# Kernel optimization log

Measured on AMD Instinct MI355X. Metric: run time of the kernel, lower is better.

Reference implementation:

```python
import jax, jax.numpy as jnp
import numpy as np

N_NODES = 100000
N_EDGES = 1600000
IN_FEATS = 256
OUT_FEATS = 128
GAMMA = 1.0


def setup_inputs() -> dict:
    key = jax.random.key(0)
    k1, k2, k3, k4, k5 = jax.random.split(key, 5)
    glorot = np.sqrt(6.0 / (IN_FEATS + OUT_FEATS)).astype(np.float32)
    feat = jax.random.normal(k1, (N_NODES, IN_FEATS), dtype=jnp.float32)
    W_mean = jax.random.uniform(k2, (IN_FEATS, OUT_FEATS), dtype=jnp.float32, minval=-glorot, maxval=glorot)
    W_var = jax.random.uniform(k3, (IN_FEATS, OUT_FEATS), dtype=jnp.float32, minval=-glorot, maxval=glorot)
    src = jax.random.randint(k4, (N_EDGES,), 0, N_NODES, dtype=jnp.int64 if jax.config.jax_enable_x64 else jnp.int32)
    dst = jax.random.randint(k5, (N_EDGES,), 0, N_NODES, dtype=jnp.int64 if jax.config.jax_enable_x64 else jnp.int32)
    return {"feat": feat, "W_mean": W_mean, "W_var": W_var, "src": src, "dst": dst}


def reference(feat, W_mean, W_var, src, dst):
    # dense projections + relu (no bias, as bias=False)
    mean = jax.nn.relu(jnp.matmul(feat, W_mean))   # [N, F]
    var = jax.nn.relu(jnp.matmul(feat, W_var))     # [N, F]
    attention = jnp.exp(-GAMMA * var)
    # in-degrees from dst edge endpoints, clamped to >= 1
    degs = jax.ops.segment_sum(jnp.ones_like(dst, dtype=jnp.float32), dst, num_segments=N_NODES)
    degs = jnp.clip(degs, 1.0)
    norm1 = (degs ** -0.5)[:, None]                # [N, 1] = D^{-1/2}
    norm2 = norm1 * norm1                          # [N, 1] = D^{-1}
    m_msg = mean * attention * norm1
    v_msg = var * attention * attention * norm2
    # copy_src + sum aggregation (SpMM over edge list)
    mean_agg = jax.ops.segment_sum(m_msg[src], dst, num_segments=N_NODES) * norm1
    var_agg = jax.ops.segment_sum(v_msg[src], dst, num_segments=N_NODES) * norm2
    return mean_agg, var_agg
```

## Files before the change

kernel.cpp:

```cpp
#include <hip/hip_runtime.h>
#include <hip/hip_bf16.h>

#define N_NODES 100000
#define N_EDGES 1600000
#define OUTF 128
#define INF 256
#define SCAN_CHUNK 1024
#define SCAN_BLOCKS 98
#define M_TILES 6250

typedef _Float16 f16;
typedef _Float16 half8 __attribute__((ext_vector_type(8)));
typedef _Float16 half2v __attribute__((ext_vector_type(2)));
typedef float floatx4 __attribute__((ext_vector_type(4)));

__global__ void count_rank_kernel(const int* __restrict__ dst, int E,
                                  int* __restrict__ deg, int* __restrict__ rank) {
    int i = blockIdx.x * blockDim.x + threadIdx.x;
    if (i < E) rank[i] = atomicAdd(&deg[dst[i]], 1);
}

__global__ __launch_bounds__(256) void scan_partial_kernel(const int* __restrict__ deg, int n,
                                                           int* __restrict__ partial) {
    __shared__ int red[256];
    int b = blockIdx.x, t = threadIdx.x;
    int base = b * SCAN_CHUNK;
    int s = 0;
    for (int i = t; i < SCAN_CHUNK; i += 256) {
        int idx = base + i;
        if (idx < n) s += deg[idx];
    }
    red[t] = s;
    __syncthreads();
    for (int off = 128; off > 0; off >>= 1) {
        if (t < off) red[t] += red[t + off];
        __syncthreads();
    }
    if (t == 0) partial[b] = red[0];
}

__global__ __launch_bounds__(128) void scan_top_kernel(int* __restrict__ partial, int nb,
                                                       int* __restrict__ row_start, int n) {
    __shared__ int sc[128];
    int t = threadIdx.x;
    int v = (t < nb) ? partial[t] : 0;
    sc[t] = v;
    __syncthreads();
    for (int off = 1; off < 128; off <<= 1) {
        int val = sc[t];
        int add = (t >= off) ? sc[t - off] : 0;
        __syncthreads();
        sc[t] = val + add;
        __syncthreads();
    }
    if (t < nb) partial[t] = sc[t] - v;
    if (t == 127) row_start[n] = sc[127];
}

__global__ __launch_bounds__(256) void scan_final_kernel(const int* __restrict__ deg, int n,
                                                         const int* __restrict__ partial,
                                                         int* __restrict__ row_start,
                                                         float* __restrict__ norm1,
                                                         float* __restrict__ norm2) {
    __shared__ int sc[256];
    int b = blockIdx.x, t = threadIdx.x;
    int base = b * SCAN_CHUNK + t * 4;
    int v[4];
    int tsum = 0;
#pragma unroll
    for (int j = 0; j < 4; j++) {
        int idx = base + j;
        v[j] = (idx < n) ? deg[idx] : 0;
        tsum += v[j];
    }
    sc[t] = tsum;
    __syncthreads();
    for (int off = 1; off < 256; off <<= 1) {
        int val = sc[t];
        int add = (t >= off) ? sc[t - off] : 0;
        __syncthreads();
        sc[t] = val + add;
        __syncthreads();
    }
    int run = sc[t] - tsum + partial[b];
#pragma unroll
    for (int j = 0; j < 4; j++) {
        int idx = base + j;
        if (idx < n) {
            row_start[idx] = run;
            float d = (float)(v[j] > 0 ? v[j] : 1);
            norm1[idx] = rsqrtf(d);
            norm2[idx] = 1.0f / d;
            run += v[j];
        }
    }
}

__global__ void scatter_edges_kernel(const int* __restrict__ src, const int* __restrict__ dst,
                                     const int* __restrict__ rank,
                                     const int* __restrict__ row_start,
                                     int E, int* __restrict__ srcs_sorted) {
    int i = blockIdx.x * blockDim.x + threadIdx.x;
    if (i < E) {
        srcs_sorted[row_start[dst[i]] + rank[i]] = src[i];
    }
}

__global__ __launch_bounds__(256) void convert_B_kernel(const float* __restrict__ Wm,
                                                        const float* __restrict__ Wv,
                                                        f16* __restrict__ Bt) {
    int k = threadIdx.x;
    int ng = blockIdx.x;
    int g = ng >> 4, i = ng & 15;
    int w = g >> 2, cg = g & 3;
    int col = w * 32 + (cg & 1) * 16 + i;
    const float* srcW = (cg >= 2) ? Wv : Wm;
    Bt[ng * 256 + k] = (f16)srcW[k * 128 + col];
}

__global__ __launch_bounds__(256, 2) void proj_mfma_kernel(const float* __restrict__ feat,
                                                           const f16* __restrict__ Bt,
                                                           const float* __restrict__ norm1,
                                                           const float* __restrict__ norm2,
                                                           f16* __restrict__ msg) {
    int tid = threadIdx.x;
    int w = tid >> 6;
    int lane = tid & 63;
    int quad = lane >> 4;
    int l15 = lane & 15;

    half8 b[4][8];
#pragma unroll
    for (int cg = 0; cg < 4; cg++) {
        int g = w * 4 + cg;
        const f16* bp = Bt + (size_t)(g * 16 + l15) * 256 + quad * 8;
#pragma unroll
        for (int kf = 0; kf < 8; kf++) {
            b[cg][kf] = *(const half8*)(bp + kf * 32);
        }
    }

    for (int t = blockIdx.x; t < M_TILES; t += gridDim.x) {
        int m0 = t * 16;
        half8 a[8];
        const float* ap = feat + (size_t)(m0 + l15) * 256 + quad * 8;
#pragma unroll
        for (int kf = 0; kf < 8; kf++) {
            floatx4 f0 = *(const floatx4*)(ap + kf * 32);
            floatx4 f1 = *(const floatx4*)(ap + kf * 32 + 4);
            half8 h;
            h[0] = (f16)f0.x; h[1] = (f16)f0.y; h[2] = (f16)f0.z; h[3] = (f16)f0.w;
            h[4] = (f16)f1.x; h[5] = (f16)f1.y; h[6] = (f16)f1.z; h[7] = (f16)f1.w;
            a[kf] = h;
        }

        floatx4 acc[4];
#pragma unroll
        for (int cg = 0; cg < 4; cg++) acc[cg] = (floatx4){0.f, 0.f, 0.f, 0.f};

#pragma unroll
        for (int cg = 0; cg < 4; cg++) {
#pragma unroll
            for (int kf = 0; kf < 8; kf++) {
                acc[cg] = __builtin_amdgcn_mfma_f32_16x16x32_f16(a[kf], b[cg][kf], acc[cg], 0, 0, 0);
            }
        }

#pragma unroll
        for (int cg = 0; cg < 2; cg++) {
            int col = w * 32 + cg * 16 + l15;
#pragma unroll
            for (int r = 0; r < 4; r++) {
                int row = quad * 4 + r;
                int node = m0 + row;
                float m = fmaxf(acc[cg][r], 0.f);
                float v = fmaxf(acc[cg + 2][r], 0.f);
                float att = __expf(-v);
                float s1 = norm1[node];
                float s2 = norm2[node];
                msg[(size_t)node * 256 + col] = (f16)(m * att * s1);
                msg[(size_t)node * 256 + 128 + col] = (f16)(v * att * att * s2);
            }
        }
    }
}

__global__ __launch_bounds__(256) void agg_kernel(const int* __restrict__ row_start,
                                                  const int* __restrict__ srcs,
                                                  const f16* __restrict__ msg,
                                                  const float* __restrict__ norm1,
                                                  const float* __restrict__ norm2,
                                                  float* __restrict__ out_mean,
                                                  float* __restrict__ out_var) {
    int d = blockIdx.x * 4 + (threadIdx.x >> 6);
    int lane = threadIdx.x & 63;
    int s0 = row_start[d];
    int s1 = row_start[d + 1];
    float am0 = 0.f, am1 = 0.f, av0 = 0.f, av1 = 0.f;
    int i = s0;
    for (; i + 3 < s1; i += 4) {
        int sa = srcs[i], sb = srcs[i + 1], sc = srcs[i + 2], sd = srcs[i + 3];
        half2v ma = *(const half2v*)(msg + (size_t)sa * 256 + lane * 2);
        half2v va = *(const half2v*)(msg + (size_t)sa * 256 + 128 + lane * 2);
        half2v mb = *(const half2v*)(msg + (size_t)sb * 256 + lane * 2);
        half2v vb = *(const half2v*)(msg + (size_t)sb * 256 + 128 + lane * 2);
        half2v mc = *(const half2v*)(msg + (size_t)sc * 256 + lane * 2);
        half2v vc = *(const half2v*)(msg + (size_t)sc * 256 + 128 + lane * 2);
        half2v md = *(const half2v*)(msg + (size_t)sd * 256 + lane * 2);
        half2v vd = *(const half2v*)(msg + (size_t)sd * 256 + 128 + lane * 2);
        am0 += (float)ma[0] + (float)mb[0] + (float)mc[0] + (float)md[0];
        am1 += (float)ma[1] + (float)mb[1] + (float)mc[1] + (float)md[1];
        av0 += (float)va[0] + (float)vb[0] + (float)vc[0] + (float)vd[0];
        av1 += (float)va[1] + (float)vb[1] + (float)vc[1] + (float)vd[1];
    }
    for (; i < s1; i++) {
        int sa = srcs[i];
        half2v ma = *(const half2v*)(msg + (size_t)sa * 256 + lane * 2);
        half2v va = *(const half2v*)(msg + (size_t)sa * 256 + 128 + lane * 2);
        am0 += (float)ma[0];
        am1 += (float)ma[1];
        av0 += (float)va[0];
        av1 += (float)va[1];
    }
    float k1 = norm1[d], k2 = norm2[d];
    float2 om = make_float2(am0 * k1, am1 * k1);
    float2 ov = make_float2(av0 * k2, av1 * k2);
    *(float2*)(out_mean + (size_t)d * 128 + lane * 2) = om;
    *(float2*)(out_var + (size_t)d * 128 + lane * 2) = ov;
}

extern "C" void kernel_launch(void* const* d_in, const int* in_sizes, int n_in,
                              void* d_out, int out_size, void* d_ws, size_t ws_size,
                              hipStream_t stream) {
    const float* feat = (const float*)d_in[0];
    const float* Wm = (const float*)d_in[1];
    const float* Wv = (const float*)d_in[2];
    const int* src = (const int*)d_in[3];
    const int* dst = (const int*)d_in[4];
    float* out = (float*)d_out;

    const int N = N_NODES;
    const int E = N_EDGES;

    char* wsp = (char*)d_ws;
    auto carve = [&](size_t bytes) {
        char* p = wsp;
        wsp += (bytes + 255) & ~(size_t)255;
        return p;
    };
    f16* msg = (f16*)carve((size_t)N * 256 * sizeof(f16));
    f16* Bt = (f16*)carve((size_t)256 * 256 * sizeof(f16));
    int* srcs_sorted = (int*)carve((size_t)E * 4);
    int* rank = (int*)carve((size_t)E * 4);
    int* deg = (int*)carve((size_t)N * 4);
    int* row_start = (int*)carve((size_t)(N + 1) * 4);
    float* norm1 = (float*)carve((size_t)N * 4);
    float* norm2 = (float*)carve((size_t)N * 4);
    int* partial = (int*)carve(128 * 4);

    hipMemsetAsync(deg, 0, (size_t)N * 4, stream);

    count_rank_kernel<<<(E + 255) / 256, 256, 0, stream>>>(dst, E, deg, rank);
    convert_B_kernel<<<256, 256, 0, stream>>>(Wm, Wv, Bt);
    scan_partial_kernel<<<SCAN_BLOCKS, 256, 0, stream>>>(deg, N, partial);
    scan_top_kernel<<<1, 128, 0, stream>>>(partial, SCAN_BLOCKS, row_start, N);
    scan_final_kernel<<<SCAN_BLOCKS, 256, 0, stream>>>(deg, N, partial, row_start, norm1, norm2);
    scatter_edges_kernel<<<(E + 255) / 256, 256, 0, stream>>>(src, dst, rank, row_start, E,
                                                              srcs_sorted);
    proj_mfma_kernel<<<1250, 256, 0, stream>>>(feat, Bt, norm1, norm2, msg);
    agg_kernel<<<N / 4, 256, 0, stream>>>(row_start, srcs_sorted, msg, norm1, norm2,
                                          out, out + (size_t)N * OUTF);
}
```

Measured before the change: 493.4 us.

## Fuse degree counting with projection and move source norms into aggregation

```diff
diff --git a/kernel.cpp b/kernel.cpp
--- a/kernel.cpp
+++ b/kernel.cpp
@@ -8,17 +8,13 @@
 #define SCAN_CHUNK 1024
 #define SCAN_BLOCKS 98
 #define M_TILES 6250
+#define E_BLOCKS 6250
 
 typedef _Float16 f16;
 typedef _Float16 half8 __attribute__((ext_vector_type(8)));
+typedef _Float16 half4 __attribute__((ext_vector_type(4)));
 typedef _Float16 half2v __attribute__((ext_vector_type(2)));
 typedef float floatx4 __attribute__((ext_vector_type(4)));
-
-__global__ void count_rank_kernel(const int* __restrict__ dst, int E,
-                                  int* __restrict__ deg, int* __restrict__ rank) {
-    int i = blockIdx.x * blockDim.x + threadIdx.x;
-    if (i < E) rank[i] = atomicAdd(&deg[dst[i]], 1);
-}
 
 __global__ __launch_bounds__(256) void scan_partial_kernel(const int* __restrict__ deg, int n,
                                                            int* __restrict__ partial) {
@@ -60,8 +56,7 @@
 __global__ __launch_bounds__(256) void scan_final_kernel(const int* __restrict__ deg, int n,
                                                          const int* __restrict__ partial,
                                                          int* __restrict__ row_start,
-                                                         float* __restrict__ norm1,
-                                                         float* __restrict__ norm2) {
+                                                         float2* __restrict__ norms) {
     __shared__ int sc[256];
     int b = blockIdx.x, t = threadIdx.x;
     int base = b * SCAN_CHUNK + t * 4;
@@ -89,8 +84,7 @@
         if (idx < n) {
             row_start[idx] = run;
             float d = (float)(v[j] > 0 ? v[j] : 1);
-            norm1[idx] = rsqrtf(d);
-            norm2[idx] = 1.0f / d;
+            norms[idx] = make_float2(rsqrtf(d), 1.0f / d);
             run += v[j];
         }
     }
@@ -118,69 +112,74 @@
     Bt[ng * 256 + k] = (f16)srcW[k * 128 + col];
 }
 
-__global__ __launch_bounds__(256, 2) void proj_mfma_kernel(const float* __restrict__ feat,
-                                                           const f16* __restrict__ Bt,
-                                                           const float* __restrict__ norm1,
-                                                           const float* __restrict__ norm2,
-                                                           f16* __restrict__ msg) {
+__global__ __launch_bounds__(256) void fused_count_proj_kernel(const int* __restrict__ dst,
+                                                               int* __restrict__ deg,
+                                                               int* __restrict__ rank,
+                                                               const float* __restrict__ feat,
+                                                               const f16* __restrict__ Bt,
+                                                               f16* __restrict__ msg) {
+    int b = blockIdx.x;
+    if ((b & 1) == 0) {
+        int i = (b >> 1) * 256 + threadIdx.x;
+        rank[i] = atomicAdd(&deg[dst[i]], 1);
+        return;
+    }
+    int t = b >> 1;
     int tid = threadIdx.x;
     int w = tid >> 6;
     int lane = tid & 63;
     int quad = lane >> 4;
     int l15 = lane & 15;
 
-    half8 b[4][8];
+    half8 bfr[4][8];
 #pragma unroll
     for (int cg = 0; cg < 4; cg++) {
         int g = w * 4 + cg;
         const f16* bp = Bt + (size_t)(g * 16 + l15) * 256 + quad * 8;
 #pragma unroll
         for (int kf = 0; kf < 8; kf++) {
-            b[cg][kf] = *(const half8*)(bp + kf * 32);
-        }
-    }
-
-    for (int t = blockIdx.x; t < M_TILES; t += gridDim.x) {
-        int m0 = t * 16;
-        half8 a[8];
-        const float* ap = feat + (size_t)(m0 + l15) * 256 + quad * 8;
+            bfr[cg][kf] = *(const half8*)(bp + kf * 32);
+        }
+    }
+
+    int m0 = t * 16;
+    half8 a[8];
+    const float* ap = feat + (size_t)(m0 + l15) * 256 + quad * 8;
+#pragma unroll
+    for (int kf = 0; kf < 8; kf++) {
+        floatx4 f0 = *(const floatx4*)(ap + kf * 32);
+        floatx4 f1 = *(const floatx4*)(ap + kf * 32 + 4);
+        half8 h;
+        h[0] = (f16)f0.x; h[1] = (f16)f0.y; h[2] = (f16)f0.z; h[3] = (f16)f0.w;
+        h[4] = (f16)f1.x; h[5] = (f16)f1.y; h[6] = (f16)f1.z; h[7] = (f16)f1.w;
+        a[kf] = h;
+    }
+
+    floatx4 acc[4];
+#pragma unroll
+    for (int cg = 0; cg < 4; cg++) acc[cg] = (floatx4){0.f, 0.f, 0.f, 0.f};
+
+#pragma unroll
+    for (int cg = 0; cg < 4; cg++) {
 #pragma unroll
         for (int kf = 0; kf < 8; kf++) {
-            floatx4 f0 = *(const floatx4*)(ap + kf * 32);
-            floatx4 f1 = *(const floatx4*)(ap + kf * 32 + 4);
-            half8 h;
-            h[0] = (f16)f0.x; h[1] = (f16)f0.y; h[2] = (f16)f0.z; h[3] = (f16)f0.w;
-            h[4] = (f16)f1.x; h[5] = (f16)f1.y; h[6] = (f16)f1.z; h[7] = (f16)f1.w;
-            a[kf] = h;
-        }
-
-        floatx4 acc[4];
-#pragma unroll
-        for (int cg = 0; cg < 4; cg++) acc[cg] = (floatx4){0.f, 0.f, 0.f, 0.f};
-
-#pragma unroll
-        for (int cg = 0; cg < 4; cg++) {
-#pragma unroll
-            for (int kf = 0; kf < 8; kf++) {
-                acc[cg] = __builtin_amdgcn_mfma_f32_16x16x32_f16(a[kf], b[cg][kf], acc[cg], 0, 0, 0);
-            }
-        }
-
-#pragma unroll
-        for (int cg = 0; cg < 2; cg++) {
-            int col = w * 32 + cg * 16 + l15;
-#pragma unroll
-            for (int r = 0; r < 4; r++) {
-                int row = quad * 4 + r;
-                int node = m0 + row;
-                float m = fmaxf(acc[cg][r], 0.f);
-                float v = fmaxf(acc[cg + 2][r], 0.f);
-                float att = __expf(-v);
-                float s1 = norm1[node];
-                float s2 = norm2[node];
-                msg[(size_t)node * 256 + col] = (f16)(m * att * s1);
-                msg[(size_t)node * 256 + 128 + col] = (f16)(v * att * att * s2);
-            }
+            acc[cg] = __builtin_amdgcn_mfma_f32_16x16x32_f16(a[kf], bfr[cg][kf], acc[cg], 0, 0, 0);
+        }
+    }
+
+#pragma unroll
+    for (int cg = 0; cg < 2; cg++) {
+        int col = w * 32 + cg * 16 + l15;
+#pragma unroll
+        for (int r = 0; r < 4; r++) {
+            int node = m0 + quad * 4 + r;
+            float m = fmaxf(acc[cg][r], 0.f);
+            float v = fmaxf(acc[cg + 2][r], 0.f);
+            float att = __expf(-v);
+            half2v mv;
+            mv[0] = (f16)(m * att);
+            mv[1] = (f16)(v * att * att);
+            *(half2v*)(msg + (size_t)node * 256 + 2 * col) = mv;
         }
     }
 }
@@ -188,8 +187,7 @@
 __global__ __launch_bounds__(256) void agg_kernel(const int* __restrict__ row_start,
                                                   const int* __restrict__ srcs,
                                                   const f16* __restrict__ msg,
-                                                  const float* __restrict__ norm1,
-                                                  const float* __restrict__ norm2,
+                                                  const float2* __restrict__ norms,
                                                   float* __restrict__ out_mean,
                                                   float* __restrict__ out_var) {
     int d = blockIdx.x * 4 + (threadIdx.x >> 6);
@@ -200,33 +198,28 @@
     int i = s0;
     for (; i + 3 < s1; i += 4) {
         int sa = srcs[i], sb = srcs[i + 1], sc = srcs[i + 2], sd = srcs[i + 3];
-        half2v ma = *(const half2v*)(msg + (size_t)sa * 256 + lane * 2);
-        half2v va = *(const half2v*)(msg + (size_t)sa * 256 + 128 + lane * 2);
-        half2v mb = *(const half2v*)(msg + (size_t)sb * 256 + lane * 2);
-        half2v vb = *(const half2v*)(msg + (size_t)sb * 256 + 128 + lane * 2);
-        half2v mc = *(const half2v*)(msg + (size_t)sc * 256 + lane * 2);
-        half2v vc = *(const half2v*)(msg + (size_t)sc * 256 + 128 + lane * 2);
-        half2v md = *(const half2v*)(msg + (size_t)sd * 256 + lane * 2);
-        half2v vd = *(const half2v*)(msg + (size_t)sd * 256 + 128 + lane * 2);
-        am0 += (float)ma[0] + (float)mb[0] + (float)mc[0] + (float)md[0];
-        am1 += (float)ma[1] + (float)mb[1] + (float)mc[1] + (float)md[1];
-        av0 += (float)va[0] + (float)vb[0] + (float)vc[0] + (float)vd[0];
-        av1 += (float)va[1] + (float)vb[1] + (float)vc[1] + (float)vd[1];
+        float2 na = norms[sa], nb = norms[sb], nc = norms[sc], nd = norms[sd];
+        half4 ha = *(const half4*)(msg + (size_t)sa * 256 + lane * 4);
+        half4 hb = *(const half4*)(msg + (size_t)sb * 256 + lane * 4);
+        half4 hc = *(const half4*)(msg + (size_t)sc * 256 + lane * 4);
+        half4 hd = *(const half4*)(msg + (size_t)sd * 256 + lane * 4);
+        am0 += (float)ha[0] * na.x + (float)hb[0] * nb.x + (float)hc[0] * nc.x + (float)hd[0] * nd.x;
+        av0 += (float)ha[1] * na.y + (float)hb[1] * nb.y + (float)hc[1] * nc.y + (float)hd[1] * nd.y;
+        am1 += (float)ha[2] * na.x + (float)hb[2] * nb.x + (float)hc[2] * nc.x + (float)hd[2] * nd.x;
+        av1 += (float)ha[3] * na.y + (float)hb[3] * nb.y + (float)hc[3] * nc.y + (float)hd[3] * nd.y;
     }
     for (; i < s1; i++) {
         int sa = srcs[i];
-        half2v ma = *(const half2v*)(msg + (size_t)sa * 256 + lane * 2);
-        half2v va = *(const half2v*)(msg + (size_t)sa * 256 + 128 + lane * 2);
-        am0 += (float)ma[0];
-        am1 += (float)ma[1];
-        av0 += (float)va[0];
-        av1 += (float)va[1];
-    }
-    float k1 = norm1[d], k2 = norm2[d];
-    float2 om = make_float2(am0 * k1, am1 * k1);
-    float2 ov = make_float2(av0 * k2, av1 * k2);
-    *(float2*)(out_mean + (size_t)d * 128 + lane * 2) = om;
-    *(float2*)(out_var + (size_t)d * 128 + lane * 2) = ov;
+        float2 na = norms[sa];
+        half4 ha = *(const half4*)(msg + (size_t)sa * 256 + lane * 4);
+        am0 += (float)ha[0] * na.x;
+        av0 += (float)ha[1] * na.y;
+        am1 += (float)ha[2] * na.x;
+        av1 += (float)ha[3] * na.y;
+    }
+    float2 nd2 = norms[d];
+    *(float2*)(out_mean + (size_t)d * 128 + lane * 2) = make_float2(am0 * nd2.x, am1 * nd2.x);
+    *(float2*)(out_var + (size_t)d * 128 + lane * 2) = make_float2(av0 * nd2.y, av1 * nd2.y);
 }
 
 extern "C" void kernel_launch(void* const* d_in, const int* in_sizes, int n_in,
@@ -254,20 +247,18 @@
     int* rank = (int*)carve((size_t)E * 4);
     int* deg = (int*)carve((size_t)N * 4);
     int* row_start = (int*)carve((size_t)(N + 1) * 4);
-    float* norm1 = (float*)carve((size_t)N * 4);
-    float* norm2 = (float*)carve((size_t)N * 4);
+    float2* norms = (float2*)carve((size_t)N * sizeof(float2));
     int* partial = (int*)carve(128 * 4);
 
     hipMemsetAsync(deg, 0, (size_t)N * 4, stream);
 
-    count_rank_kernel<<<(E + 255) / 256, 256, 0, stream>>>(dst, E, deg, rank);
     convert_B_kernel<<<256, 256, 0, stream>>>(Wm, Wv, Bt);
+    fused_count_proj_kernel<<<E_BLOCKS + M_TILES, 256, 0, stream>>>(dst, deg, rank, feat, Bt, msg);
     scan_partial_kernel<<<SCAN_BLOCKS, 256, 0, stream>>>(deg, N, partial);
     scan_top_kernel<<<1, 128, 0, stream>>>(partial, SCAN_BLOCKS, row_start, N);
-    scan_final_kernel<<<SCAN_BLOCKS, 256, 0, stream>>>(deg, N, partial, row_start, norm1, norm2);
+    scan_final_kernel<<<SCAN_BLOCKS, 256, 0, stream>>>(deg, N, partial, row_start, norms);
     scatter_edges_kernel<<<(E + 255) / 256, 256, 0, stream>>>(src, dst, rank, row_start, E,
                                                               srcs_sorted);
-    proj_mfma_kernel<<<1250, 256, 0, stream>>>(feat, Bt, norm1, norm2, msg);
-    agg_kernel<<<N / 4, 256, 0, stream>>>(row_start, srcs_sorted, msg, norm1, norm2,
+    agg_kernel<<<N / 4, 256, 0, stream>>>(row_start, srcs_sorted, msg, norms,
                                           out, out + (size_t)N * OUTF);
 }
```

Result: slower. 609.5 us (+23.5%).
